# Performance work log

Measured on AMD Instinct MI355X. Metric: run time of the kernel, lower is better.

## Reference

```python
import jax, jax.numpy as jnp
import numpy as np

N = 100_000
E = 1_600_000
IN_DIM = 21
HID = 256
OUT = 256


def setup_inputs() -> dict:
    key = jax.random.key(0)
    ks = jax.random.split(key, 10)
    node_scalar = jax.random.normal(ks[0], (N, IN_DIM), dtype=jnp.float32)
    edge_index = jax.random.randint(ks[1], (2, E), 0, N, dtype=jnp.int64)
    s_in = 1.0 / np.sqrt(IN_DIM)
    s_h = 1.0 / np.sqrt(HID)
    W_in = jax.random.uniform(ks[2], (IN_DIM, HID), jnp.float32, -s_in, s_in)
    b_in = jax.random.uniform(ks[3], (HID,), jnp.float32, -s_in, s_in)
    W_self = jax.random.uniform(ks[4], (HID, HID), jnp.float32, -s_h, s_h)
    b_self = jax.random.uniform(ks[5], (HID,), jnp.float32, -s_h, s_h)
    W_nei = jax.random.uniform(ks[6], (HID, HID), jnp.float32, -s_h, s_h)
    b_nei = jax.random.uniform(ks[7], (HID,), jnp.float32, -s_h, s_h)
    W_out = jax.random.uniform(ks[8], (HID, OUT), jnp.float32, -s_h, s_h)
    b_out = jax.random.uniform(ks[9], (OUT,), jnp.float32, -s_h, s_h)
    return {
        "node_scalar": node_scalar,
        "W_in": W_in, "b_in": b_in,
        "W_self": W_self, "b_self": b_self,
        "W_nei": W_nei, "b_nei": b_nei,
        "W_out": W_out, "b_out": b_out,
        "edge_index": edge_index,
    }


def reference(node_scalar, W_in, b_in, W_self, b_self, W_nei, b_nei, W_out, b_out, edge_index):
    # x = relu(Linear(node_scalar)); dropout is identity in eval mode
    x = jax.nn.relu(node_scalar @ W_in + b_in)           # (N, H)
    n = x.shape[0]
    src, dst = edge_index[0], edge_index[1]
    msg = x[src]                                          # (E, H) gather
    agg = jax.ops.segment_sum(msg, dst, num_segments=n)   # (N, H) scatter-add
    deg = jax.ops.segment_sum(jnp.ones((dst.shape[0],), dtype=x.dtype), dst, num_segments=n)
    agg = agg / jnp.maximum(deg, 1.0)[:, None]            # degree mean (clamp_min 1)
    h = jax.nn.relu(x @ W_self + b_self + agg @ W_nei + b_nei)
    g = h.mean(axis=0)                                    # global mean pool -> (H,)
    return g @ W_out + b_out                              # (OUT,)
```

## Files before the change

kernel.cpp:

```cpp
#include <hip/hip_runtime.h>
#include <hip/hip_bf16.h>

#define HID 256
#define IND 21
#define PB 6400
#define MAXB 512

typedef short short8 __attribute__((ext_vector_type(8)));
typedef float floatx16 __attribute__((ext_vector_type(16)));
typedef float floatx2 __attribute__((ext_vector_type(2)));

__device__ inline unsigned short f2bf(float f) {
  __hip_bfloat16 h = __float2bfloat16(f);
  union { __hip_bfloat16 h; unsigned short u; } c;
  c.h = h;
  return c.u;
}

__device__ inline unsigned int pk_bf16_trunc(floatx2 p) {
  union { float f; unsigned int u; } a, b;
  a.f = p.x; b.f = p.y;
  return (b.u & 0xffff0000u) | (a.u >> 16);
}

__device__ inline void acc8p(uint2 v, floatx2* a) {
  a[0] += __builtin_amdgcn_cvt_pk_f32_fp8((int)v.x, false);
  a[1] += __builtin_amdgcn_cvt_pk_f32_fp8((int)v.x, true);
  a[2] += __builtin_amdgcn_cvt_pk_f32_fp8((int)v.y, false);
  a[3] += __builtin_amdgcn_cvt_pk_f32_fp8((int)v.y, true);
}

__device__ inline short8 mk_s8(unsigned a, unsigned b, unsigned c, unsigned d) {
  union { uint4 u; short8 s; } x; x.u = make_uint4(a, b, c, d); return x.s;
}

__device__ inline short8 dec8(uint2 v) {
  unsigned w0 = pk_bf16_trunc(__builtin_amdgcn_cvt_pk_f32_fp8((int)v.x, false));
  unsigned w1 = pk_bf16_trunc(__builtin_amdgcn_cvt_pk_f32_fp8((int)v.x, true));
  unsigned w2 = pk_bf16_trunc(__builtin_amdgcn_cvt_pk_f32_fp8((int)v.y, false));
  unsigned w3 = pk_bf16_trunc(__builtin_amdgcn_cvt_pk_f32_fp8((int)v.y, true));
  return mk_s8(w0, w1, w2, w3);
}

__device__ inline void gl16(const unsigned char* g, unsigned char* l) {
  __builtin_amdgcn_global_load_lds(
      (const __attribute__((address_space(1))) unsigned char*)g,
      (__attribute__((address_space(3))) unsigned char*)l, 16, 0, 0);
}

__global__ __launch_bounds__(256) void k_front(
    const float* __restrict__ ns, const float* __restrict__ Win,
    const float* __restrict__ bin, uint2* __restrict__ xq2,
    uint2* __restrict__ Aqx,
    const float* __restrict__ Wself, const float* __restrict__ Wnei,
    unsigned short* __restrict__ Bf16,
    const int* __restrict__ dst, int* __restrict__ bcnt,
    int N, int E, int nb2, int G1) {
  int blk = blockIdx.x;
  int tid = threadIdx.x;
  if (blk < G1) {
    __shared__ __align__(16) float s[8][24];
    __shared__ float fx[8][257];
    int nb = blk * 8;
    if (tid < 8 * IND) {
      int idx = nb * IND + tid;
      s[tid / IND][tid % IND] = (idx < N * IND) ? ns[idx] : 0.f;
    }
    float w[IND];
#pragma unroll
    for (int k = 0; k < IND; k++) w[k] = Win[k * HID + tid];
    float b = bin[tid];
    __syncthreads();
#pragma unroll
    for (int j = 0; j < 8; j++) {
      float acc = b;
      const float4* sp = (const float4*)&s[j][0];
#pragma unroll
      for (int k4 = 0; k4 < 5; k4++) {
        float4 t = sp[k4];
        acc += t.x * w[k4 * 4] + t.y * w[k4 * 4 + 1] +
               t.z * w[k4 * 4 + 2] + t.w * w[k4 * 4 + 3];
      }
      acc += s[j][20] * w[20];
      fx[j][tid] = acc > 0.f ? acc : 0.f;
    }
    __syncthreads();
    {
      int j = tid & 7, u = tid >> 3;
      int node = nb + j;
      if (node < N) {
        const float* fp = &fx[j][u * 8];
        int lo0 = __builtin_amdgcn_cvt_pk_fp8_f32(fp[0], fp[1], 0, false);
        int w0  = __builtin_amdgcn_cvt_pk_fp8_f32(fp[2], fp[3], lo0, true);
        int lo1 = __builtin_amdgcn_cvt_pk_fp8_f32(fp[4], fp[5], 0, false);
        int w1  = __builtin_amdgcn_cvt_pk_fp8_f32(fp[6], fp[7], lo1, true);
        uint2 val = make_uint2((unsigned)w0, (unsigned)w1);
        xq2[(size_t)node * 32 + u] = val;
        int g = node >> 5, row = node & 31, c = u >> 1, hi = u & 1;
        Aqx[(size_t)(g * 16 + c) * 64 + hi * 32 + row] = val;
      }
    }
  } else if (blk < G1 + 256) {
    int n = blk - G1;
    int ct = n >> 5, l5 = n & 31;
#pragma unroll
    for (int t = 0; t < 2; t++) {
      int k = tid + t * 256;
      float v = (k < HID) ? Wself[k * HID + n] : Wnei[(k - HID) * HID + n];
      int c = k >> 4, kin = k & 15;
      int lane = (kin >> 3) * 32 + l5;
      int j = kin & 7;
      Bf16[(size_t)((c * 8 + ct) * 64 + lane) * 8 + j] = f2bf(v);
    }
  } else {
    __shared__ int lh[MAXB];
    int e0 = (blk - G1 - 256) * PB;
    for (int b = tid; b < nb2; b += 256) lh[b] = 0;
    __syncthreads();
    int c = min(PB, E - e0);
    for (int i = tid; i < c; i += 256) atomicAdd(&lh[dst[e0 + i] >> 8], 1);
    __syncthreads();
    for (int b = tid; b < nb2; b += 256)
      if (lh[b]) atomicAdd(&bcnt[b], lh[b]);
  }
}

__global__ __launch_bounds__(512) void k_bscan(
    const int* __restrict__ bcnt, int* __restrict__ bbase, int* __restrict__ bcur,
    int* __restrict__ row_start, int E, int N, int nb2) {
  __shared__ int ts[512];
  int tid = threadIdx.x;
  int v = (tid < nb2) ? bcnt[tid] : 0;
  ts[tid] = v;
  __syncthreads();
  for (int off = 1; off < 512; off <<= 1) {
    int t = (tid >= off) ? ts[tid - off] : 0;
    __syncthreads();
    ts[tid] += t;
    __syncthreads();
  }
  if (tid < nb2) { bbase[tid] = ts[tid] - v; bcur[tid] = ts[tid] - v; }
  if (tid == 0) { bbase[nb2] = E; row_start[N] = E; }
}

__global__ __launch_bounds__(256) void k_part(
    const int* __restrict__ src, const int* __restrict__ dst,
    int* __restrict__ bcur, unsigned int* __restrict__ ebuf, int E, int nb2) {
  __shared__ int lh[MAXB];
  int tid = threadIdx.x;
  int e0 = blockIdx.x * PB;
  for (int b = tid; b < nb2; b += 256) lh[b] = 0;
  __syncthreads();
  int cnt = min(PB, E - e0);
  for (int i = tid; i < cnt; i += 256) atomicAdd(&lh[dst[e0 + i] >> 8], 1);
  __syncthreads();
  for (int b = tid; b < nb2; b += 256) {
    int c = lh[b];
    lh[b] = (c > 0) ? atomicAdd(&bcur[b], c) : 0;
  }
  __syncthreads();
  for (int i = tid; i < cnt; i += 256) {
    int s = src[e0 + i];
    int d = dst[e0 + i];
    int pos = atomicAdd(&lh[d >> 8], 1);
    ebuf[pos] = ((unsigned)s << 8) | ((unsigned)d & 255u);
  }
}

__global__ __launch_bounds__(256) void k_fill2(
    const unsigned int* __restrict__ ebuf, const int* __restrict__ bbase,
    int* __restrict__ row_start, unsigned int* __restrict__ csr, int N) {
  __shared__ int lcnt[256];
  __shared__ int lcur[256];
  __shared__ int ts[256];
  int b = blockIdx.x;
  int tid = threadIdx.x;
  int start = bbase[b], end = bbase[b + 1];
  lcnt[tid] = 0;
  __syncthreads();
  for (int i = start + tid; i < end; i += 256)
    atomicAdd(&lcnt[ebuf[i] & 255u], 1);
  __syncthreads();
  int v = lcnt[tid];
  ts[tid] = v;
  __syncthreads();
  for (int off = 1; off < 256; off <<= 1) {
    int t = (tid >= off) ? ts[tid - off] : 0;
    __syncthreads();
    ts[tid] += t;
    __syncthreads();
  }
  int excl = start + ts[tid] - v;
  int node = (b << 8) + tid;
  if (node < N) row_start[node] = excl;
  lcur[tid] = excl;
  __syncthreads();
  for (int i = start + tid; i < end; i += 256) {
    unsigned int e = ebuf[i];
    int pos = atomicAdd(&lcur[e & 255u], 1);
    csr[pos] = e & ~255u;
  }
}

__global__ __launch_bounds__(256) void k_agg(
    const unsigned char* __restrict__ xqb, const unsigned int* __restrict__ csrb,
    const int* __restrict__ row_start, uint2* __restrict__ Aqagg, int N, int n0) {
  __shared__ uint2 ld[8][33];
  int tid = threadIdx.x;
  int lane = tid & 63;
  int w = tid >> 6;
  int half = lane >> 5;
  int l32 = lane & 31;
  unsigned lo = (unsigned)(l32 * 8);

  int nl = w * 2 + half;
  int wid = n0 + blockIdx.x * 8 + nl;
  int cw = (wid < N) ? wid : (N - 1);
  int start = row_start[cw];
  int end = row_start[cw + 1];
  int c = end - start;
  floatx2 a[4], b[4], d[4], e[4];
#pragma unroll
  for (int j = 0; j < 4; j++) {
    a[j] = (floatx2){0.f, 0.f}; b[j] = (floatx2){0.f, 0.f};
    d[j] = (floatx2){0.f, 0.f}; e[j] = (floatx2){0.f, 0.f};
  }
  int i = 0;
  while (i < c) {
    int nb = min(32, c - i);
    int sel = (l32 < nb) ? l32 : 0;
    unsigned idx = csrb[start + i + sel];
    int j = 0;
    for (; j + 8 <= nb; j += 8) {
      unsigned o0 = (unsigned)__shfl((int)idx, j + 0, 32) + lo;
      unsigned o1 = (unsigned)__shfl((int)idx, j + 1, 32) + lo;
      unsigned o2 = (unsigned)__shfl((int)idx, j + 2, 32) + lo;
      unsigned o3 = (unsigned)__shfl((int)idx, j + 3, 32) + lo;
      unsigned o4 = (unsigned)__shfl((int)idx, j + 4, 32) + lo;
      unsigned o5 = (unsigned)__shfl((int)idx, j + 5, 32) + lo;
      unsigned o6 = (unsigned)__shfl((int)idx, j + 6, 32) + lo;
      unsigned o7 = (unsigned)__shfl((int)idx, j + 7, 32) + lo;
      uint2 v0 = *(const uint2*)(xqb + o0);
      uint2 v1 = *(const uint2*)(xqb + o1);
      uint2 v2 = *(const uint2*)(xqb + o2);
      uint2 v3 = *(const uint2*)(xqb + o3);
      uint2 v4 = *(const uint2*)(xqb + o4);
      uint2 v5 = *(const uint2*)(xqb + o5);
      uint2 v6 = *(const uint2*)(xqb + o6);
      uint2 v7 = *(const uint2*)(xqb + o7);
      acc8p(v0, a); acc8p(v1, b); acc8p(v2, d); acc8p(v3, e);
      acc8p(v4, a); acc8p(v5, b); acc8p(v6, d); acc8p(v7, e);
    }
    for (; j + 4 <= nb; j += 4) {
      unsigned o0 = (unsigned)__shfl((int)idx, j + 0, 32) + lo;
      unsigned o1 = (unsigned)__shfl((int)idx, j + 1, 32) + lo;
      unsigned o2 = (unsigned)__shfl((int)idx, j + 2, 32) + lo;
      unsigned o3 = (unsigned)__shfl((int)idx, j + 3, 32) + lo;
      uint2 v0 = *(const uint2*)(xqb + o0);
      uint2 v1 = *(const uint2*)(xqb + o1);
      uint2 v2 = *(const uint2*)(xqb + o2);
      uint2 v3 = *(const uint2*)(xqb + o3);
      acc8p(v0, a); acc8p(v1, b); acc8p(v2, d); acc8p(v3, e);
    }
    for (; j < nb; j++) {
      unsigned o0 = (unsigned)__shfl((int)idx, j, 32) + lo;
      uint2 v0 = *(const uint2*)(xqb + o0);
      acc8p(v0, a);
    }
    i += nb;
  }
#pragma unroll
  for (int j = 0; j < 4; j++) a[j] += b[j] + d[j] + e[j];

  float inv = 1.0f / fmaxf((float)c, 1.0f);
  float f[8];
#pragma unroll
  for (int j = 0; j < 4; j++) {
    f[2 * j] = a[j].x * inv;
    f[2 * j + 1] = a[j].y * inv;
  }
  int lo0 = __builtin_amdgcn_cvt_pk_fp8_f32(f[0], f[1], 0, false);
  int w0  = __builtin_amdgcn_cvt_pk_fp8_f32(f[2], f[3], lo0, true);
  int lo1 = __builtin_amdgcn_cvt_pk_fp8_f32(f[4], f[5], 0, false);
  int w1  = __builtin_amdgcn_cvt_pk_fp8_f32(f[6], f[7], lo1, true);
  ld[nl][l32] = make_uint2((unsigned)w0, (unsigned)w1);
  __syncthreads();

  int g = (n0 >> 5) + (blockIdx.x >> 2);
  int r0 = (blockIdx.x & 3) * 8;
  int s = tid >> 3, j = tid & 7;
  Aqagg[(size_t)g * 1024 + (size_t)s * 32 + r0 + j] = ld[j][s];
}

__global__ __launch_bounds__(256, 4) void k_h(
    const unsigned char* __restrict__ Aqx, const unsigned char* __restrict__ Aqagg,
    const unsigned char* __restrict__ Bf8, const float* __restrict__ bself,
    const float* __restrict__ bnei, float* __restrict__ gsum, int N, int nfull) {
  __shared__ __align__(16) unsigned char As[2][8192];
  __shared__ float colsum[128];
  int bid = blockIdx.x;
  int bx, by;
  if (bid < nfull) {
    bx = (bid >> 4) * 8 + (bid & 7);
    by = (bid >> 3) & 1;
  } else {
    int rem = bid - nfull;
    bx = (nfull >> 1) + (rem >> 1);
    by = rem & 1;
  }
  int tid = threadIdx.x;
  int lane = tid & 63;
  int w = tid >> 6;
  int wr = w >> 1, wc = w & 1;
  int l32 = lane & 31, half = lane >> 5;
  int rowBase = bx * 128;

  if (tid < 128) colsum[tid] = 0.f;

  floatx16 acc[2][2];
#pragma unroll
  for (int i = 0; i < 2; i++)
#pragma unroll
    for (int j = 0; j < 2; j++) acc[i][j] = (floatx16)(0.f);

  size_t a_grp = (size_t)(bx * 4 + w) * 16 * 512;
  int lb = lane * 16;

  {
    const unsigned char* asrc = Aqx + a_grp + lb;
    gl16(asrc, As[0] + w * 2048);
    gl16(asrc + 1024, As[0] + w * 2048 + 1024);
  }

  for (int ch = 0; ch < 8; ch++) {
    int buf = ch & 1;
    __syncthreads();
    if (ch < 7) {
      int cn = ch + 1;
      const unsigned char* Aq = (cn < 4) ? Aqx : Aqagg;
      const unsigned char* asrc = Aq + a_grp + (size_t)(cn & 3) * 2048 + lb;
      unsigned char* ad = As[buf ^ 1] + w * 2048;
      gl16(asrc, ad);
      gl16(asrc + 1024, ad + 1024);
    }
#pragma unroll
    for (int cl = 0; cl < 4; cl++) {
      short8 afr[2];
#pragma unroll
      for (int rt = 0; rt < 2; rt++) {
        uint2 av = *(const uint2*)&As[buf][(wr * 2 + rt) * 2048 + cl * 512 + lane * 8];
        afr[rt] = dec8(av);
      }
#pragma unroll
      for (int ctw = 0; ctw < 2; ctw++) {
        int cfull = ch * 4 + cl;
        int ctg = by * 4 + wc * 2 + ctw;
        short8 bfr = *(const short8*)(
            Bf8 + ((size_t)(cfull * 8 + ctg) * 64 + lane) * 16);
#pragma unroll
        for (int rt = 0; rt < 2; rt++)
          acc[rt][ctw] = __builtin_amdgcn_mfma_f32_32x32x16_bf16(
              afr[rt], bfr, acc[rt][ctw], 0, 0, 0);
      }
    }
  }

#pragma unroll
  for (int ctw = 0; ctw < 2; ctw++) {
    int lcol = (wc * 2 + ctw) * 32 + l32;
    int gcol = by * 128 + lcol;
    float bb = bself[gcol] + bnei[gcol];
    float psum = 0.f;
#pragma unroll
    for (int rt = 0; rt < 2; rt++) {
#pragma unroll
      for (int r = 0; r < 16; r++) {
        int rw = rowBase + wr * 64 + rt * 32 + (r & 3) + 8 * (r >> 2) + 4 * half;
        float v = acc[rt][ctw][r] + bb;
        v = v > 0.f ? v : 0.f;
        if (rw < N) psum += v;
      }
    }
    atomicAdd(&colsum[lcol], psum);
  }
  __syncthreads();
  if (tid < 128) atomicAdd(&gsum[by * 128 + tid], colsum[tid]);
}

__global__ __launch_bounds__(HID) void k_out(
    const float* __restrict__ gsum, const float* __restrict__ Wout,
    const float* __restrict__ bout, float* __restrict__ out, float invN) {
  __shared__ float g[HID];
  int c = threadIdx.x;
  g[c] = gsum[c] * invN;
  __syncthreads();
  float acc = bout[c];
#pragma unroll 8
  for (int k = 0; k < HID; k++) acc += g[k] * Wout[k * HID + c];
  out[c] = acc;
}

extern "C" void kernel_launch(void* const* d_in, const int* in_sizes, int n_in,
                              void* d_out, int out_size, void* d_ws, size_t ws_size,
                              hipStream_t stream) {
  const float* ns    = (const float*)d_in[0];
  const float* Win   = (const float*)d_in[1];
  const float* bin   = (const float*)d_in[2];
  const float* Wself = (const float*)d_in[3];
  const float* bself = (const float*)d_in[4];
  const float* Wnei  = (const float*)d_in[5];
  const float* bnei  = (const float*)d_in[6];
  const float* Wout  = (const float*)d_in[7];
  const float* bout  = (const float*)d_in[8];
  const int*   eidx  = (const int*)d_in[9];

  int N = in_sizes[0] / IND;
  int E = in_sizes[9] / 2;
  const int* src = eidx;
  const int* dst = eidx + E;
  int nb2 = (N + 255) >> 8;
  int nbx = (N + 127) / 128;
  size_t NGU = (size_t)nbx * 4 * 16 * 64;

  unsigned int* xq     = (unsigned int*)d_ws;
  uint2* Aqx           = (uint2*)(xq + (size_t)N * 64);
  uint2* Aqagg         = Aqx + NGU;
  unsigned short* Bf16 = (unsigned short*)(Aqagg + NGU);
  unsigned int* csr  = (unsigned int*)(Bf16 + 256 * 512);
  unsigned int* ebuf = csr + E;
  int* row_start = (int*)(ebuf + E);
  int* bcnt      = row_start + N + 1;
  float* gsum    = (float*)(bcnt + MAXB);
  int* bbase     = (int*)(gsum + HID);
  int* bcur      = bbase + MAXB + 1;

  hipMemsetAsync(bcnt, 0, (MAXB + HID) * sizeof(int), stream);

  int G1 = (N + 7) / 8;
  int pgrid = (E + PB - 1) / PB;
  k_front<<<G1 + 256 + pgrid, 256, 0, stream>>>(
      ns, Win, bin, (uint2*)xq, Aqx, Wself, Wnei, Bf16, dst, bcnt,
      N, E, nb2, G1);

  k_bscan<<<1, 512, 0, stream>>>(bcnt, bbase, bcur, row_start, E, N, nb2);
  k_part<<<pgrid, 256, 0, stream>>>(src, dst, bcur, ebuf, E, nb2);
  k_fill2<<<nb2, 256, 0, stream>>>(ebuf, bbase, row_start, csr, N);

  int H = (((N / 2) + 31) / 32) * 32;
  if (H > N) H = N;
  int agrid1 = H / 8;
  int agrid2 = (N - H + 7) / 8;
  if (agrid1 > 0)
    k_agg<<<agrid1, 256, 0, stream>>>((const unsigned char*)xq, csr, row_start,
                                      Aqagg, N, 0);
  if (agrid2 > 0)
    k_agg<<<agrid2, 256, 0, stream>>>((const unsigned char*)xq, csr, row_start,
                                      Aqagg, N, H);

  int nblocks = nbx * 2;
  int nfull = (nblocks / 16) * 16;
  k_h<<<nblocks, 256, 0, stream>>>((const unsigned char*)Aqx,
                                   (const unsigned char*)Aqagg,
                                   (const unsigned char*)Bf16,
                                   bself, bnei, gsum, N, nfull);

  k_out<<<1, HID, 0, stream>>>(gsum, Wout, bout, (float*)d_out, 1.0f / (float)N);
}
```

Before: 282.0 us.

## Load A fragments directly from global in k_h, dropping LDS staging

```diff
diff --git a/kernel.cpp b/kernel.cpp
--- a/kernel.cpp
+++ b/kernel.cpp
@@ -40,12 +40,6 @@
   unsigned w2 = pk_bf16_trunc(__builtin_amdgcn_cvt_pk_f32_fp8((int)v.y, false));
   unsigned w3 = pk_bf16_trunc(__builtin_amdgcn_cvt_pk_f32_fp8((int)v.y, true));
   return mk_s8(w0, w1, w2, w3);
-}
-
-__device__ inline void gl16(const unsigned char* g, unsigned char* l) {
-  __builtin_amdgcn_global_load_lds(
-      (const __attribute__((address_space(1))) unsigned char*)g,
-      (__attribute__((address_space(3))) unsigned char*)l, 16, 0, 0);
 }
 
 __global__ __launch_bounds__(256) void k_front(
@@ -292,11 +286,10 @@
   Aqagg[(size_t)g * 1024 + (size_t)s * 32 + r0 + j] = ld[j][s];
 }
 
-__global__ __launch_bounds__(256, 4) void k_h(
+__global__ __launch_bounds__(256, 3) void k_h(
     const unsigned char* __restrict__ Aqx, const unsigned char* __restrict__ Aqagg,
     const unsigned char* __restrict__ Bf8, const float* __restrict__ bself,
     const float* __restrict__ bnei, float* __restrict__ gsum, int N, int nfull) {
-  __shared__ __align__(16) unsigned char As[2][8192];
   __shared__ float colsum[128];
   int bid = blockIdx.x;
   int bx, by;
@@ -323,48 +316,29 @@
 #pragma unroll
     for (int j = 0; j < 2; j++) acc[i][j] = (floatx16)(0.f);
 
-  size_t a_grp = (size_t)(bx * 4 + w) * 16 * 512;
-  int lb = lane * 16;
-
-  {
-    const unsigned char* asrc = Aqx + a_grp + lb;
-    gl16(asrc, As[0] + w * 2048);
-    gl16(asrc + 1024, As[0] + w * 2048 + 1024);
-  }
+  size_t agrp = (size_t)(bx * 4 + wr * 2) * 8192 + (size_t)(lane * 8);
+  size_t bgrp = ((size_t)(by * 4 + wc * 2) * 64 + lane) * 16;
 
   for (int ch = 0; ch < 8; ch++) {
-    int buf = ch & 1;
-    __syncthreads();
-    if (ch < 7) {
-      int cn = ch + 1;
-      const unsigned char* Aq = (cn < 4) ? Aqx : Aqagg;
-      const unsigned char* asrc = Aq + a_grp + (size_t)(cn & 3) * 2048 + lb;
-      unsigned char* ad = As[buf ^ 1] + w * 2048;
-      gl16(asrc, ad);
-      gl16(asrc + 1024, ad + 1024);
-    }
+    const unsigned char* Aq = (ch < 4) ? Aqx : Aqagg;
+    const unsigned char* abase = Aq + agrp + (size_t)(ch & 3) * 2048;
 #pragma unroll
     for (int cl = 0; cl < 4; cl++) {
-      short8 afr[2];
-#pragma unroll
-      for (int rt = 0; rt < 2; rt++) {
-        uint2 av = *(const uint2*)&As[buf][(wr * 2 + rt) * 2048 + cl * 512 + lane * 8];
-        afr[rt] = dec8(av);
-      }
-#pragma unroll
-      for (int ctw = 0; ctw < 2; ctw++) {
-        int cfull = ch * 4 + cl;
-        int ctg = by * 4 + wc * 2 + ctw;
-        short8 bfr = *(const short8*)(
-            Bf8 + ((size_t)(cfull * 8 + ctg) * 64 + lane) * 16);
-#pragma unroll
-        for (int rt = 0; rt < 2; rt++)
-          acc[rt][ctw] = __builtin_amdgcn_mfma_f32_32x32x16_bf16(
-              afr[rt], bfr, acc[rt][ctw], 0, 0, 0);
-      }
-    }
-  }
-
+      uint2 a0 = *(const uint2*)(abase + cl * 512);
+      uint2 a1 = *(const uint2*)(abase + 8192 + cl * 512);
+      const unsigned char* bbase = Bf8 + bgrp + (size_t)(ch * 4 + cl) * 8192;
+      short8 b0 = *(const short8*)(bbase);
+      short8 b1 = *(const short8*)(bbase + 1024);
+      short8 af0 = dec8(a0);
+      short8 af1 = dec8(a1);
+      acc[0][0] = __builtin_amdgcn_mfma_f32_32x32x16_bf16(af0, b0, acc[0][0], 0, 0, 0);
+      acc[1][0] = __builtin_amdgcn_mfma_f32_32x32x16_bf16(af1, b0, acc[1][0], 0, 0, 0);
+      acc[0][1] = __builtin_amdgcn_mfma_f32_32x32x16_bf16(af0, b1, acc[0][1], 0, 0, 0);
+      acc[1][1] = __builtin_amdgcn_mfma_f32_32x32x16_bf16(af1, b1, acc[1][1], 0, 0, 0);
+    }
+  }
+
+  __syncthreads();
 #pragma unroll
   for (int ctw = 0; ctw < 2; ctw++) {
     int lcol = (wc * 2 + ctw) * 32 + l32;
```

New measurement: 287.5 us. No clear change (+1.9%).
